# Optimization experiments

Hardware: AMD Instinct MI355X
Metric: run time of the kernel (lower is better)

Reference implementation:

```python
import jax, jax.numpy as jnp
import numpy as np

N = 20000      # nodes
E = 50000      # edges
B = 128        # graphs in batch
H = 64         # hidden_dim
FEAT = 28      # raw node feature dim
N_TYPES = 100  # one-hot size for node_type
EDGE_DIM = 5   # one-hot size for edge_type
OUT = 1        # output_dim
MP_ITER = 3
S2S_ITER = 4


def setup_inputs() -> dict:
    key = jax.random.key(0)
    ks = jax.random.split(key, 24)
    s = 0.05
    inp = {
        'node_feat': jax.random.normal(ks[0], (N, FEAT), dtype=jnp.float32),
        'node_type': jax.random.randint(ks[1], (N,), 0, N_TYPES),
        'edge_index': jax.random.randint(ks[2], (2, E), 0, N),
        'edge_type': jax.random.randint(ks[3], (E,), 0, EDGE_DIM),
        'batch': jnp.sort(jax.random.randint(ks[4], (N,), 0, B)),
        # node embedding
        'W_emb': jax.random.normal(ks[5], (N_TYPES + FEAT, H), dtype=jnp.float32) * s,
        'b_emb': jnp.zeros((H,), dtype=jnp.float32),
        # shared edge net: edge_dim -> H -> H*H
        'W_e1': jax.random.normal(ks[6], (EDGE_DIM, H), dtype=jnp.float32) * s,
        'b_e1': jnp.zeros((H,), dtype=jnp.float32),
        'W_e2': jax.random.normal(ks[7], (H, H * H), dtype=jnp.float32) * s,
        'b_e2': jnp.zeros((H * H,), dtype=jnp.float32),
        # per-layer NNConv root weight + bias
        'roots': jax.random.normal(ks[8], (MP_ITER, H, H), dtype=jnp.float32) * s,
        'conv_bias': jnp.zeros((MP_ITER, H), dtype=jnp.float32),
        # Set2Set LSTM (input 2H, hidden H); torch gate order i,f,g,o
        'W_ih': jax.random.normal(ks[9], (4 * H, 2 * H), dtype=jnp.float32) * s,
        'W_hh': jax.random.normal(ks[10], (4 * H, H), dtype=jnp.float32) * s,
        'b_ih': jnp.zeros((4 * H,), dtype=jnp.float32),
        'b_hh': jnp.zeros((4 * H,), dtype=jnp.float32),
        # output MLP 2H -> H -> OUT
        'W_o1': jax.random.normal(ks[11], (2 * H, H), dtype=jnp.float32) * s,
        'b_o1': jnp.zeros((H,), dtype=jnp.float32),
        'W_o2': jax.random.normal(ks[12], (H, OUT), dtype=jnp.float32) * s,
        'b_o2': jnp.zeros((OUT,), dtype=jnp.float32),
    }
    return inp


def _forward(node_feat, W_emb, b_emb, W_e1, b_e1, W_e2, b_e2, roots, conv_bias,
             W_ih, W_hh, b_ih, b_hh, W_o1, b_o1, W_o2, b_o2,
             node_type, edge_index, edge_type, batch):
    # node embedding: [one_hot(node_type,100) ; node_feat] @ W_emb
    x_in = jnp.concatenate(
        [jax.nn.one_hot(node_type, N_TYPES, dtype=node_feat.dtype), node_feat], axis=-1)
    h = x_in @ W_emb + b_emb                                   # [N, H]

    # edge-conditioned weights (edge_attr is fixed, edge_net is shared across
    # iterations, so nn(edge_attr) is identical each layer -> compute once)
    edge_attr = jax.nn.one_hot(edge_type, EDGE_DIM, dtype=node_feat.dtype)
    Wmat = jax.nn.relu(edge_attr @ W_e1 + b_e1) @ W_e2 + b_e2  # [E, H*H]
    Wmat = Wmat.reshape(E, H, H)                               # [E, H_in, H_out]

    src, dst = edge_index[0], edge_index[1]
    for i in range(MP_ITER):
        msg = jnp.einsum('eh,eho->eo', h[src], Wmat)           # per-edge matvec
        agg = jax.ops.segment_sum(msg, dst, num_segments=N)    # sum aggregation
        h = agg + h @ roots[i] + conv_bias[i]                  # NNConv root + bias

    # Set2Set pooling
    hx = jnp.zeros((B, H), dtype=h.dtype)
    cx = jnp.zeros((B, H), dtype=h.dtype)
    q_star = jnp.zeros((B, 2 * H), dtype=h.dtype)
    for _ in range(S2S_ITER):
        gates = q_star @ W_ih.T + b_ih + hx @ W_hh.T + b_hh
        ig, fg, gg, og = jnp.split(gates, 4, axis=-1)
        cx = jax.nn.sigmoid(fg) * cx + jax.nn.sigmoid(ig) * jnp.tanh(gg)
        hx = jax.nn.sigmoid(og) * jnp.tanh(cx)
        q = hx                                                 # [B, H]
        e = jnp.sum(h * q[batch], axis=-1)                     # [N]
        m = jax.lax.stop_gradient(jax.ops.segment_max(e, batch, num_segments=B))
        a = jnp.exp(e - m[batch])
        denom = jax.ops.segment_sum(a, batch, num_segments=B)
        denom = jnp.where(denom == 0, 1.0, denom)
        a = a / denom[batch]                                   # scatter softmax
        r = jax.ops.segment_sum(a[:, None] * h, batch, num_segments=B)  # [B, H]
        q_star = jnp.concatenate([q, r], axis=-1)

    out = jax.nn.relu(q_star @ W_o1 + b_o1) @ W_o2 + b_o2      # [B, OUT]
    return out


def reference(node_feat, node_type, edge_index, edge_type, batch,
              W_emb, b_emb, W_e1, b_e1, W_e2, b_e2, roots, conv_bias,
              W_ih, W_hh, b_ih, b_hh, W_o1, b_o1, W_o2, b_o2):
    return _forward(node_feat, W_emb, b_emb, W_e1, b_e1, W_e2, b_e2, roots,
                    conv_bias, W_ih, W_hh, b_ih, b_hh, W_o1, b_o1, W_o2, b_o2,
                    node_type, edge_index, edge_type, batch)
```

## Files before the change

### kernel.cpp

```cpp
#include <hip/hip_runtime.h>
#include <math.h>


#define NN 20000
#define NE 50000
#define NB 128
#define HD 64
#define NFEAT 28
#define NTYPES 100
#define EDIM 5
#define MPIT 3
#define S2SIT 4
#define NBLK_E ((NE + 255) / 256)
#define SMAX 224
#define HP (HD + 1)

__device__ __forceinline__ float sigm(float x) {
  return 1.0f / (1.0f + expf(-x));
}

__global__ __launch_bounds__(256) void k_starts(
    const int* __restrict__ batch, int* __restrict__ gstart) {
  int n = blockIdx.x * blockDim.x + threadIdx.x;
  if (n >= NN) return;
  int b = batch[n];
  if (n == 0)
    for (int t = 0; t <= b; ++t) gstart[t] = 0;
  int bn = (n + 1 < NN) ? batch[n + 1] : NB;
  for (int t = b + 1; t <= bn; ++t) gstart[t] = n + 1;
}

__global__ __launch_bounds__(256) void k_setup(
    const float* __restrict__ feat, const int* __restrict__ ntype,
    const int* __restrict__ etype,
    const float* __restrict__ W_emb, const float* __restrict__ b_emb,
    const float* __restrict__ W_e1, const float* __restrict__ b_e1,
    const float* __restrict__ W_e2, const float* __restrict__ b_e2,
    const float* __restrict__ W_ih, const float* __restrict__ W_hh,
    float* __restrict__ Wty, float* __restrict__ hA,
    float* __restrict__ W_ihT, float* __restrict__ W_hhT,
    int* __restrict__ bc) {
  __shared__ int wcc[4][EDIM];
  __shared__ float sv[EDIM][HD];
  __shared__ float red[4][EDIM][HD];
  const int tid = threadIdx.x;
  const int lane = tid & 63;
  const int wv = tid >> 6;
  const int blk = blockIdx.x;
  const int nblk = gridDim.x;
  const int nthr = nblk << 8;
  const int gtid = (blk << 8) + tid;
  const int gw = (blk << 2) + wv;
  const int nwave = nblk << 2;

  if (blk < NBLK_E) {
    int e = (blk << 8) + tid;
    int ty = (e < NE) ? etype[e] : -1;
    #pragma unroll
    for (int t = 0; t < EDIM; ++t) {
      unsigned long long m = __ballot(ty == t);
      if (lane == 0) wcc[wv][t] = __popcll(m);
    }
    __syncthreads();
    if (tid < EDIM)
      bc[blk * EDIM + tid] = wcc[0][tid] + wcc[1][tid] + wcc[2][tid] + wcc[3][tid];
    __syncthreads();
  }

  if (blk >= NBLK_E && blk < NBLK_E + 64) {
    int mbase = (blk - NBLK_E) * 64;
    for (int idx = tid; idx < EDIM * HD; idx += 256) {
      int t = idx >> 6, j = idx & 63;
      float x = W_e1[t * HD + j] + b_e1[j];
      sv[t][j] = x > 0.f ? x : 0.f;
    }
    __syncthreads();
    int l = tid & 63, jg = tid >> 6;
    float acc[EDIM] = {0.f, 0.f, 0.f, 0.f, 0.f};
    #pragma unroll
    for (int jj = 0; jj < 16; ++jj) {
      int j = jg * 16 + jj;
      float w2 = W_e2[j * 4096 + mbase + l];
      #pragma unroll
      for (int t = 0; t < EDIM; ++t) acc[t] = fmaf(sv[t][j], w2, acc[t]);
    }
    #pragma unroll
    for (int t = 0; t < EDIM; ++t) red[jg][t][l] = acc[t];
    __syncthreads();
    for (int idx = tid; idx < EDIM * HD; idx += 256) {
      int t = idx >> 6, m = idx & 63;
      float s = red[0][t][m] + red[1][t][m] + red[2][t][m] + red[3][t][m];
      Wty[t * 4096 + mbase + m] = s + b_e2[mbase + m];
    }
  }

  for (int o = gtid; o < 2 * HD * 4 * HD; o += nthr)
    W_ihT[o] = W_ih[(o & 255) * 128 + (o >> 8)];
  for (int o = gtid; o < HD * 4 * HD; o += nthr)
    W_hhT[o] = W_hh[(o & 255) * 64 + (o >> 8)];

  {
    float wf[NFEAT];
    #pragma unroll
    for (int f = 0; f < NFEAT; ++f) wf[f] = W_emb[(NTYPES + f) * HD + lane];
    float bb = b_emb[lane];
    for (int n = gw; n < NN; n += nwave) {
      int nu = __builtin_amdgcn_readfirstlane(n);
      int t = __builtin_amdgcn_readfirstlane(ntype[nu]);
      const float* row = feat + nu * NFEAT;
      float acc = bb + W_emb[t * HD + lane];
      #pragma unroll
      for (int f = 0; f < NFEAT; ++f) acc = fmaf(row[f], wf[f], acc);
      hA[nu * HD + lane] = acc;
    }
  }
}

__global__ __launch_bounds__(256) void k_place(
    const int* __restrict__ etype, const int* __restrict__ ei,
    const int* __restrict__ bc,
    int2* __restrict__ sd, int* __restrict__ offs_out) {
  __shared__ int s_base[EDIM];
  __shared__ int wc[4][EDIM];
  const int tid = threadIdx.x;
  const int lane = tid & 63;
  const int wv = tid >> 6;
  const int blk = blockIdx.x;

  if (wv == 0) {
    int part[EDIM], tot[EDIM];
    #pragma unroll
    for (int t = 0; t < EDIM; ++t) { part[t] = 0; tot[t] = 0; }
    for (int b = lane; b < NBLK_E; b += 64) {
      #pragma unroll
      for (int t = 0; t < EDIM; ++t) {
        int x = bc[b * EDIM + t];
        tot[t] += x;
        if (b < blk) part[t] += x;
      }
    }
    #pragma unroll
    for (int t = 0; t < EDIM; ++t) {
      #pragma unroll
      for (int off = 32; off; off >>= 1) {
        tot[t]  += __shfl_xor(tot[t],  off, 64);
        part[t] += __shfl_xor(part[t], off, 64);
      }
    }
    if (lane == 0) {
      int run = 0;
      #pragma unroll
      for (int t = 0; t < EDIM; ++t) {
        s_base[t] = run + part[t];
        if (blk == 0) offs_out[t] = run;
        run += tot[t];
      }
      if (blk == 0) offs_out[EDIM] = run;
    }
  }

  int e = (blk << 8) + tid;
  int ty = (e < NE) ? etype[e] : -1;
  int sv = 0, dv = 0;
  if (e < NE) { sv = ei[e]; dv = ei[NE + e]; }
  int rank = 0;
  #pragma unroll
  for (int t = 0; t < EDIM; ++t) {
    unsigned long long m = __ballot(ty == t);
    if (lane == 0) wc[wv][t] = __popcll(m);
    if (ty == t) rank = __popcll(m & ((1ull << lane) - 1ull));
  }
  __syncthreads();
  if (ty >= 0) {
    int base = s_base[ty];
    for (int w = 0; w < wv; ++w) base += wc[w][ty];
    sd[base + rank] = make_int2(sv, dv);
  }
}

__global__ __launch_bounds__(256) void k_root(
    const float* __restrict__ h, float* __restrict__ hnext,
    const float* __restrict__ root, const float* __restrict__ bias) {
  const int lane = threadIdx.x & 63;
  const int wid = __builtin_amdgcn_readfirstlane(blockIdx.x * 4 + (threadIdx.x >> 6));
  const int nw = gridDim.x * 4;
  float w[HD];
  #pragma unroll
  for (int k = 0; k < HD; ++k) w[k] = root[k * HD + lane];
  float bb = bias[lane];
  for (int n = wid; n < NN; n += nw) {
    const float* row = h + n * HD;
    float a0 = 0.f, a1 = 0.f, a2 = 0.f, a3 = 0.f;
    #pragma unroll
    for (int k = 0; k < HD; k += 4) {
      a0 = fmaf(row[k + 0], w[k + 0], a0);
      a1 = fmaf(row[k + 1], w[k + 1], a1);
      a2 = fmaf(row[k + 2], w[k + 2], a2);
      a3 = fmaf(row[k + 3], w[k + 3], a3);
    }
    hnext[n * HD + lane] = bb + ((a0 + a1) + (a2 + a3));
  }
}

__global__ __launch_bounds__(256) void k_msg(
    const int2* __restrict__ sd, const int* __restrict__ offs_in,
    const float* __restrict__ Wty, const float* __restrict__ hsrc,
    float* __restrict__ htgt) {
  const int lane = threadIdx.x & 63;
  const int wv = threadIdx.x >> 6;
  int wid = (blockIdx.x << 2) + wv;
  const int nw = 8192;
  int per = (NE + nw - 1) / nw;
  int beg = wid * per;
  int end = beg + per; if (end > NE) end = NE;
  if (beg >= end) return;
  int offs[EDIM + 1];
  #pragma unroll
  for (int t = 0; t <= EDIM; ++t) offs[t] = offs_in[t];
  for (int t = 0; t < EDIM; ++t) {
    int lo = offs[t];     if (lo < beg) lo = beg;
    int hi = offs[t + 1]; if (hi > end) hi = end;
    if (lo >= hi) continue;
    float w[HD];
    #pragma unroll
    for (int k = 0; k < HD; ++k) w[k] = Wty[t * 4096 + k * HD + lane];
    for (int p = lo; p < hi; ++p) {
      int2 e = sd[p];
      int s = __builtin_amdgcn_readfirstlane(e.x);
      int d = __builtin_amdgcn_readfirstlane(e.y);
      const float* row = hsrc + s * HD;
      float a0 = 0.f, a1 = 0.f, a2 = 0.f, a3 = 0.f;
      #pragma unroll
      for (int k = 0; k < HD; k += 4) {
        a0 = fmaf(row[k + 0], w[k + 0], a0);
        a1 = fmaf(row[k + 1], w[k + 1], a1);
        a2 = fmaf(row[k + 2], w[k + 2], a2);
        a3 = fmaf(row[k + 3], w[k + 3], a3);
      }
      atomicAdd(&htgt[d * HD + lane], (a0 + a1) + (a2 + a3));
    }
  }
}

__global__ __launch_bounds__(256) void k_s2s(
    const float* __restrict__ h, const int* __restrict__ gstart,
    const float* __restrict__ W_ihT, const float* __restrict__ W_hhT,
    const float* __restrict__ b_ih, const float* __restrict__ b_hh,
    const float* __restrict__ W_o1, const float* __restrict__ b_o1,
    const float* __restrict__ W_o2, const float* __restrict__ b_o2,
    float* __restrict__ out) {
  __shared__ float hs[SMAX * HP];
  __shared__ float ebuf[SMAX];
  __shared__ float qstar[2 * HD];
  __shared__ float hxs[HD], cxs[HD], gates[4 * HD];
  __shared__ float redM[4], redS[4], redR[4][HD];
  __shared__ float hid[HD];
  int b = blockIdx.x;
  int tid = threadIdx.x;
  int lane = tid & 63, wv = tid >> 6;

  int st = gstart[b], en = gstart[b + 1];
  int cnt = en - st;
  int cached = cnt < SMAX ? cnt : SMAX;

  int total = cached * HD;
  for (int base = tid * 4; base < total; base += 1024) {
    float4 v = *reinterpret_cast<const float4*>(h + st * HD + base);
    int n = base >> 6, k = base & 63;
    float* row = hs + n * HP + k;
    row[0] = v.x; row[1] = v.y; row[2] = v.z; row[3] = v.w;
  }
  if (tid < 2 * HD) qstar[tid] = 0.f;
  if (tid < HD) { hxs[tid] = 0.f; cxs[tid] = 0.f; }
  __syncthreads();

  for (int it = 0; it < S2SIT; ++it) {
    float acc0 = b_ih[tid] + b_hh[tid], acc1 = 0.f;
    #pragma unroll 8
    for (int j = 0; j < 2 * HD; j += 2) {
      acc0 = fmaf(qstar[j],     W_ihT[j * 256 + tid],       acc0);
      acc1 = fmaf(qstar[j + 1], W_ihT[(j + 1) * 256 + tid], acc1);
    }
    #pragma unroll 8
    for (int j = 0; j < HD; j += 2) {
      acc0 = fmaf(hxs[j],     W_hhT[j * 256 + tid],       acc0);
      acc1 = fmaf(hxs[j + 1], W_hhT[(j + 1) * 256 + tid], acc1);
    }
    gates[tid] = acc0 + acc1;
    __syncthreads();
    if (tid < HD) {
      float ig = sigm(gates[tid]);
      float fg = sigm(gates[HD + tid]);
      float gg = tanhf(gates[2 * HD + tid]);
      float og = sigm(gates[3 * HD + tid]);
      float c = fmaf(fg, cxs[tid], ig * gg);
      cxs[tid] = c;
      hxs[tid] = og * tanhf(c);
    }
    __syncthreads();

    float e = -1e30f;
    if (tid < cached) {
      const float* row = hs + tid * HP;
      float d0 = 0.f, d1 = 0.f;
      #pragma unroll 8
      for (int k = 0; k < HD; k += 2) {
        d0 = fmaf(row[k],     hxs[k],     d0);
        d1 = fmaf(row[k + 1], hxs[k + 1], d1);
      }
      e = d0 + d1;
      ebuf[tid] = e;
    }
    float m = e;
    #pragma unroll
    for (int off = 32; off; off >>= 1) m = fmaxf(m, __shfl_xor(m, off, 64));
    float qreg = hxs[lane];
    for (int n = cached + wv; n < cnt; n += 4) {
      float ev = h[(st + n) * HD + lane] * qreg;
      #pragma unroll
      for (int off = 32; off; off >>= 1) ev += __shfl_xor(ev, off, 64);
      m = fmaxf(m, ev);
    }
    if (lane == 0) redM[wv] = m;
    __syncthreads();
    float M = fmaxf(fmaxf(redM[0], redM[1]), fmaxf(redM[2], redM[3]));

    float sp = 0.f;
    if (tid < cached) {
      float a = expf(ebuf[tid] - M);
      ebuf[tid] = a;
      sp = a;
    }
    #pragma unroll
    for (int off = 32; off; off >>= 1) sp += __shfl_xor(sp, off, 64);
    __syncthreads();

    float r = 0.f;
    for (int n = wv; n < cached; n += 4)
      r = fmaf(ebuf[n], hs[n * HP + lane], r);
    float s_tail = 0.f;
    for (int n = cached + wv; n < cnt; n += 4) {
      float v = h[(st + n) * HD + lane];
      float ev = v * qreg;
      #pragma unroll
      for (int off = 32; off; off >>= 1) ev += __shfl_xor(ev, off, 64);
      float a = expf(ev - M);
      s_tail += a;
      r = fmaf(a, v, r);
    }
    if (lane == 0) redS[wv] = sp + s_tail;
    redR[wv][lane] = r;
    __syncthreads();
    if (tid < HD) {
      float S = redS[0] + redS[1] + redS[2] + redS[3];
      float R = redR[0][tid] + redR[1][tid] + redR[2][tid] + redR[3][tid];
      if (S == 0.f) S = 1.f;
      qstar[tid] = hxs[tid];
      qstar[HD + tid] = R / S;
    }
    __syncthreads();
  }

  if (tid < HD) {
    float acc = b_o1[tid];
    #pragma unroll 8
    for (int i = 0; i < 2 * HD; ++i)
      acc = fmaf(qstar[i], W_o1[i * HD + tid], acc);
    hid[tid] = acc > 0.f ? acc : 0.f;
  }
  __syncthreads();
  if (tid < HD) {
    float p = hid[tid] * W_o2[tid];
    #pragma unroll
    for (int off = 32; off; off >>= 1) p += __shfl_xor(p, off, 64);
    if (tid == 0) out[b] = p + b_o2[0];
  }
}

extern "C" void kernel_launch(void* const* d_in, const int* in_sizes, int n_in,
                              void* d_out, int out_size, void* d_ws, size_t ws_size,
                              hipStream_t stream) {
  const float* node_feat = (const float*)d_in[0];
  const int*   node_type = (const int*)d_in[1];
  const int*   edge_index= (const int*)d_in[2];
  const int*   edge_type = (const int*)d_in[3];
  const int*   batch     = (const int*)d_in[4];
  const float* W_emb     = (const float*)d_in[5];
  const float* b_emb     = (const float*)d_in[6];
  const float* W_e1      = (const float*)d_in[7];
  const float* b_e1      = (const float*)d_in[8];
  const float* W_e2      = (const float*)d_in[9];
  const float* b_e2      = (const float*)d_in[10];
  const float* roots     = (const float*)d_in[11];
  const float* conv_bias = (const float*)d_in[12];
  const float* W_ih      = (const float*)d_in[13];
  const float* W_hh      = (const float*)d_in[14];
  const float* b_ih      = (const float*)d_in[15];
  const float* b_hh      = (const float*)d_in[16];
  const float* W_o1      = (const float*)d_in[17];
  const float* b_o1      = (const float*)d_in[18];
  const float* W_o2      = (const float*)d_in[19];
  const float* b_o2      = (const float*)d_in[20];
  float* out = (float*)d_out;

  float* Wty   = (float*)d_ws;
  float* hA    = Wty + EDIM * 4096;
  float* hB    = hA + NN * HD;
  float* W_ihT = hB + NN * HD;
  float* W_hhT = W_ihT + 2 * HD * 4 * HD;
  int2*  sd    = (int2*)(W_hhT + HD * 4 * HD);
  int*   gstart= (int*)(sd + NE);
  int*   bc    = gstart + 136;
  int*   offs  = bc + NBLK_E * EDIM;

  k_starts<<<(NN + 255) / 256, 256, 0, stream>>>(batch, gstart);
  k_setup<<<512, 256, 0, stream>>>(node_feat, node_type, edge_type,
                                   W_emb, b_emb, W_e1, b_e1, W_e2, b_e2,
                                   W_ih, W_hh, Wty, hA, W_ihT, W_hhT, bc);
  k_place<<<NBLK_E, 256, 0, stream>>>(edge_type, edge_index, bc, sd, offs);

  const float* hcur = hA;
  float* hnxt = hB;
  for (int i = 0; i < MPIT; ++i) {
    k_root<<<512, 256, 0, stream>>>(hcur, hnxt, roots + i * HD * HD,
                                    conv_bias + i * HD);
    k_msg<<<2048, 256, 0, stream>>>(sd, offs, Wty, hcur, hnxt);
    const float* tmp = hnxt; hnxt = (float*)hcur; hcur = tmp;
  }

  k_s2s<<<NB, 256, 0, stream>>>(hcur, gstart, W_ihT, W_hhT, b_ih, b_hh,
                                W_o1, b_o1, W_o2, b_o2, out);
}
```

Baseline: 240.2 us.

## Sort edges by destination and fuse root transform with message aggregation in LDS

Replaces the edge-type bucketing with a destination-sorted CSR built from a degree count, a single-block scan and an atomic placement pass. Each message-passing block owns 16 destination nodes and accumulates messages in shared memory with LDS atomics. It then adds the root transform and bias in the same kernel, which removes global atomics and one launch per layer. The cost is that each wave rescans its edge range once per edge type and reloads the weight registers per type, and the placement pass adds a serial one-block scan. The packed source index uses 16 bits, which relies on N fitting in that range.

```diff
diff --git a/kernel.cpp b/kernel.cpp
--- a/kernel.cpp
+++ b/kernel.cpp
@@ -11,7 +11,8 @@
 #define EDIM 5
 #define MPIT 3
 #define S2SIT 4
-#define NBLK_E ((NE + 255) / 256)
+#define RNG 16
+#define NBLK_MP (NN / RNG)
 #define SMAX 224
 #define HP (HD + 1)
 
@@ -20,9 +21,12 @@
 }
 
 __global__ __launch_bounds__(256) void k_starts(
-    const int* __restrict__ batch, int* __restrict__ gstart) {
+    const int* __restrict__ batch, int* __restrict__ gstart,
+    int* __restrict__ dcnt, int* __restrict__ dcur) {
   int n = blockIdx.x * blockDim.x + threadIdx.x;
   if (n >= NN) return;
+  dcnt[n] = 0;
+  dcur[n] = 0;
   int b = batch[n];
   if (n == 0)
     for (int t = 0; t <= b; ++t) gstart[t] = 0;
@@ -32,15 +36,14 @@
 
 __global__ __launch_bounds__(256) void k_setup(
     const float* __restrict__ feat, const int* __restrict__ ntype,
-    const int* __restrict__ etype,
+    const int* __restrict__ ei,
     const float* __restrict__ W_emb, const float* __restrict__ b_emb,
     const float* __restrict__ W_e1, const float* __restrict__ b_e1,
     const float* __restrict__ W_e2, const float* __restrict__ b_e2,
     const float* __restrict__ W_ih, const float* __restrict__ W_hh,
     float* __restrict__ Wty, float* __restrict__ hA,
     float* __restrict__ W_ihT, float* __restrict__ W_hhT,
-    int* __restrict__ bc) {
-  __shared__ int wcc[4][EDIM];
+    int* __restrict__ dcnt) {
   __shared__ float sv[EDIM][HD];
   __shared__ float red[4][EDIM][HD];
   const int tid = threadIdx.x;
@@ -53,22 +56,8 @@
   const int gw = (blk << 2) + wv;
   const int nwave = nblk << 2;
 
-  if (blk < NBLK_E) {
-    int e = (blk << 8) + tid;
-    int ty = (e < NE) ? etype[e] : -1;
-    #pragma unroll
-    for (int t = 0; t < EDIM; ++t) {
-      unsigned long long m = __ballot(ty == t);
-      if (lane == 0) wcc[wv][t] = __popcll(m);
-    }
-    __syncthreads();
-    if (tid < EDIM)
-      bc[blk * EDIM + tid] = wcc[0][tid] + wcc[1][tid] + wcc[2][tid] + wcc[3][tid];
-    __syncthreads();
-  }
-
-  if (blk >= NBLK_E && blk < NBLK_E + 64) {
-    int mbase = (blk - NBLK_E) * 64;
+  if (blk < 64) {
+    int mbase = blk * 64;
     for (int idx = tid; idx < EDIM * HD; idx += 256) {
       int t = idx >> 6, j = idx & 63;
       float x = W_e1[t * HD + j] + b_e1[j];
@@ -114,120 +103,89 @@
       hA[nu * HD + lane] = acc;
     }
   }
-}
-
-__global__ __launch_bounds__(256) void k_place(
-    const int* __restrict__ etype, const int* __restrict__ ei,
-    const int* __restrict__ bc,
-    int2* __restrict__ sd, int* __restrict__ offs_out) {
-  __shared__ int s_base[EDIM];
-  __shared__ int wc[4][EDIM];
+
+  for (int e = gtid; e < NE; e += nthr)
+    atomicAdd(&dcnt[ei[NE + e]], 1);
+}
+
+__global__ __launch_bounds__(1024) void k_dscan(
+    const int* __restrict__ dcnt, int* __restrict__ dstart) {
+  __shared__ int buf[1024];
+  const int tid = threadIdx.x;
+  const int CH = 20;
+  int base = tid * CH;
+  int loc[CH];
+  int s = 0;
+  #pragma unroll
+  for (int i = 0; i < CH; ++i) {
+    int n = base + i;
+    loc[i] = (n < NN) ? dcnt[n] : 0;
+    s += loc[i];
+  }
+  buf[tid] = s;
+  __syncthreads();
+  for (int off = 1; off < 1024; off <<= 1) {
+    int x = (tid >= off) ? buf[tid - off] : 0;
+    __syncthreads();
+    buf[tid] += x;
+    __syncthreads();
+  }
+  int run = buf[tid] - s;
+  #pragma unroll
+  for (int i = 0; i < CH; ++i) {
+    int n = base + i;
+    if (n < NN) dstart[n] = run;
+    run += loc[i];
+  }
+  if (tid == 1023) dstart[NN] = run;
+}
+
+__global__ __launch_bounds__(256) void k_placeD(
+    const int* __restrict__ ei, const int* __restrict__ etype,
+    const int* __restrict__ dstart, int* __restrict__ dcur,
+    int2* __restrict__ sdD) {
+  int e = blockIdx.x * 256 + threadIdx.x;
+  if (e >= NE) return;
+  int s = ei[e], d = ei[NE + e], t = etype[e];
+  int r = atomicAdd(&dcur[d], 1);
+  sdD[dstart[d] + r] = make_int2(s | (t << 16), d);
+}
+
+__global__ __launch_bounds__(256) void k_mp(
+    const int2* __restrict__ sdD, const int* __restrict__ dstart,
+    const float* __restrict__ Wty, const float* __restrict__ hsrc,
+    float* __restrict__ htgt,
+    const float* __restrict__ root, const float* __restrict__ bias) {
+  __shared__ float tile[RNG * HD];
   const int tid = threadIdx.x;
   const int lane = tid & 63;
   const int wv = tid >> 6;
-  const int blk = blockIdx.x;
-
-  if (wv == 0) {
-    int part[EDIM], tot[EDIM];
-    #pragma unroll
-    for (int t = 0; t < EDIM; ++t) { part[t] = 0; tot[t] = 0; }
-    for (int b = lane; b < NBLK_E; b += 64) {
-      #pragma unroll
-      for (int t = 0; t < EDIM; ++t) {
-        int x = bc[b * EDIM + t];
-        tot[t] += x;
-        if (b < blk) part[t] += x;
+  const int nbase = blockIdx.x * RNG;
+
+  for (int i = tid; i < RNG * HD; i += 256) tile[i] = 0.f;
+  int lo = dstart[nbase];
+  int hi = dstart[nbase + RNG];
+  __syncthreads();
+
+  int len = hi - lo;
+  int per = (len + 3) >> 2;
+  int mylo = lo + wv * per;
+  int myhi = mylo + per; if (myhi > hi) myhi = hi;
+
+  float w[HD];
+  for (int t = 0; t < EDIM; ++t) {
+    bool wl = false;
+    for (int p = mylo; p < myhi; ++p) {
+      int ex = __builtin_amdgcn_readfirstlane(sdD[p].x);
+      int ty = ex >> 16;
+      if (ty != t) continue;
+      if (!wl) {
+        #pragma unroll
+        for (int k = 0; k < HD; ++k) w[k] = Wty[t * 4096 + k * HD + lane];
+        wl = true;
       }
-    }
-    #pragma unroll
-    for (int t = 0; t < EDIM; ++t) {
-      #pragma unroll
-      for (int off = 32; off; off >>= 1) {
-        tot[t]  += __shfl_xor(tot[t],  off, 64);
-        part[t] += __shfl_xor(part[t], off, 64);
-      }
-    }
-    if (lane == 0) {
-      int run = 0;
-      #pragma unroll
-      for (int t = 0; t < EDIM; ++t) {
-        s_base[t] = run + part[t];
-        if (blk == 0) offs_out[t] = run;
-        run += tot[t];
-      }
-      if (blk == 0) offs_out[EDIM] = run;
-    }
-  }
-
-  int e = (blk << 8) + tid;
-  int ty = (e < NE) ? etype[e] : -1;
-  int sv = 0, dv = 0;
-  if (e < NE) { sv = ei[e]; dv = ei[NE + e]; }
-  int rank = 0;
-  #pragma unroll
-  for (int t = 0; t < EDIM; ++t) {
-    unsigned long long m = __ballot(ty == t);
-    if (lane == 0) wc[wv][t] = __popcll(m);
-    if (ty == t) rank = __popcll(m & ((1ull << lane) - 1ull));
-  }
-  __syncthreads();
-  if (ty >= 0) {
-    int base = s_base[ty];
-    for (int w = 0; w < wv; ++w) base += wc[w][ty];
-    sd[base + rank] = make_int2(sv, dv);
-  }
-}
-
-__global__ __launch_bounds__(256) void k_root(
-    const float* __restrict__ h, float* __restrict__ hnext,
-    const float* __restrict__ root, const float* __restrict__ bias) {
-  const int lane = threadIdx.x & 63;
-  const int wid = __builtin_amdgcn_readfirstlane(blockIdx.x * 4 + (threadIdx.x >> 6));
-  const int nw = gridDim.x * 4;
-  float w[HD];
-  #pragma unroll
-  for (int k = 0; k < HD; ++k) w[k] = root[k * HD + lane];
-  float bb = bias[lane];
-  for (int n = wid; n < NN; n += nw) {
-    const float* row = h + n * HD;
-    float a0 = 0.f, a1 = 0.f, a2 = 0.f, a3 = 0.f;
-    #pragma unroll
-    for (int k = 0; k < HD; k += 4) {
-      a0 = fmaf(row[k + 0], w[k + 0], a0);
-      a1 = fmaf(row[k + 1], w[k + 1], a1);
-      a2 = fmaf(row[k + 2], w[k + 2], a2);
-      a3 = fmaf(row[k + 3], w[k + 3], a3);
-    }
-    hnext[n * HD + lane] = bb + ((a0 + a1) + (a2 + a3));
-  }
-}
-
-__global__ __launch_bounds__(256) void k_msg(
-    const int2* __restrict__ sd, const int* __restrict__ offs_in,
-    const float* __restrict__ Wty, const float* __restrict__ hsrc,
-    float* __restrict__ htgt) {
-  const int lane = threadIdx.x & 63;
-  const int wv = threadIdx.x >> 6;
-  int wid = (blockIdx.x << 2) + wv;
-  const int nw = 8192;
-  int per = (NE + nw - 1) / nw;
-  int beg = wid * per;
-  int end = beg + per; if (end > NE) end = NE;
-  if (beg >= end) return;
-  int offs[EDIM + 1];
-  #pragma unroll
-  for (int t = 0; t <= EDIM; ++t) offs[t] = offs_in[t];
-  for (int t = 0; t < EDIM; ++t) {
-    int lo = offs[t];     if (lo < beg) lo = beg;
-    int hi = offs[t + 1]; if (hi > end) hi = end;
-    if (lo >= hi) continue;
-    float w[HD];
-    #pragma unroll
-    for (int k = 0; k < HD; ++k) w[k] = Wty[t * 4096 + k * HD + lane];
-    for (int p = lo; p < hi; ++p) {
-      int2 e = sd[p];
-      int s = __builtin_amdgcn_readfirstlane(e.x);
-      int d = __builtin_amdgcn_readfirstlane(e.y);
+      int s = ex & 0xFFFF;
+      int d = __builtin_amdgcn_readfirstlane(sdD[p].y);
       const float* row = hsrc + s * HD;
       float a0 = 0.f, a1 = 0.f, a2 = 0.f, a3 = 0.f;
       #pragma unroll
@@ -237,8 +195,28 @@
         a2 = fmaf(row[k + 2], w[k + 2], a2);
         a3 = fmaf(row[k + 3], w[k + 3], a3);
       }
-      atomicAdd(&htgt[d * HD + lane], (a0 + a1) + (a2 + a3));
-    }
+      atomicAdd(&tile[(d - nbase) * HD + lane], (a0 + a1) + (a2 + a3));
+    }
+  }
+  __syncthreads();
+
+  #pragma unroll
+  for (int k = 0; k < HD; ++k) w[k] = root[k * HD + lane];
+  float bb = bias[lane];
+  #pragma unroll
+  for (int i = 0; i < RNG / 4; ++i) {
+    int dl = wv * (RNG / 4) + i;
+    int n = nbase + dl;
+    const float* row = hsrc + n * HD;
+    float a0 = bb, a1 = 0.f, a2 = 0.f, a3 = 0.f;
+    #pragma unroll
+    for (int k = 0; k < HD; k += 4) {
+      a0 = fmaf(row[k + 0], w[k + 0], a0);
+      a1 = fmaf(row[k + 1], w[k + 1], a1);
+      a2 = fmaf(row[k + 2], w[k + 2], a2);
+      a3 = fmaf(row[k + 3], w[k + 3], a3);
+    }
+    htgt[n * HD + lane] = ((a0 + a1) + (a2 + a3)) + tile[dl * HD + lane];
   }
 }
 
@@ -408,23 +386,25 @@
   float* hB    = hA + NN * HD;
   float* W_ihT = hB + NN * HD;
   float* W_hhT = W_ihT + 2 * HD * 4 * HD;
-  int2*  sd    = (int2*)(W_hhT + HD * 4 * HD);
-  int*   gstart= (int*)(sd + NE);
-  int*   bc    = gstart + 136;
-  int*   offs  = bc + NBLK_E * EDIM;
-
-  k_starts<<<(NN + 255) / 256, 256, 0, stream>>>(batch, gstart);
-  k_setup<<<512, 256, 0, stream>>>(node_feat, node_type, edge_type,
+  int2*  sdD   = (int2*)(W_hhT + HD * 4 * HD);
+  int*   gstart= (int*)(sdD + NE);
+  int*   dcnt  = gstart + 136;
+  int*   dcur  = dcnt + NN;
+  int*   dstart= dcur + NN;
+
+  k_starts<<<(NN + 255) / 256, 256, 0, stream>>>(batch, gstart, dcnt, dcur);
+  k_setup<<<512, 256, 0, stream>>>(node_feat, node_type, edge_index,
                                    W_emb, b_emb, W_e1, b_e1, W_e2, b_e2,
-                                   W_ih, W_hh, Wty, hA, W_ihT, W_hhT, bc);
-  k_place<<<NBLK_E, 256, 0, stream>>>(edge_type, edge_index, bc, sd, offs);
+                                   W_ih, W_hh, Wty, hA, W_ihT, W_hhT, dcnt);
+  k_dscan<<<1, 1024, 0, stream>>>(dcnt, dstart);
+  k_placeD<<<(NE + 255) / 256, 256, 0, stream>>>(edge_index, edge_type,
+                                                 dstart, dcur, sdD);
 
   const float* hcur = hA;
   float* hnxt = hB;
   for (int i = 0; i < MPIT; ++i) {
-    k_root<<<512, 256, 0, stream>>>(hcur, hnxt, roots + i * HD * HD,
-                                    conv_bias + i * HD);
-    k_msg<<<2048, 256, 0, stream>>>(sd, offs, Wty, hcur, hnxt);
+    k_mp<<<NBLK_MP, 256, 0, stream>>>(sdD, dstart, Wty, hcur, hnxt,
+                                      roots + i * HD * HD, conv_bias + i * HD);
     const float* tmp = hnxt; hnxt = (float*)hcur; hcur = tmp;
   }
 
```

After: 329.3 us. +37.1%, slower.
